# Performance work log

Measured on AMD Instinct MI355X. Metric: run time of the kernel, lower is better.

## Reference

```python
import jax, jax.numpy as jnp
import numpy as np

N, E = 100000, 1600000
IN_DIM, H, D = 128, 4, 32
ALPHA = 0.2  # leaky relu negative slope


def setup_inputs() -> dict:
    key = jax.random.key(0)
    k1, k2, k3, k4, k5, k6 = jax.random.split(key, 6)
    return {
        "inputs": jax.random.normal(k1, (N, IN_DIM), dtype=jnp.float32),
        "src": jax.random.randint(k2, (E,), 0, N, dtype=jnp.int32),
        "dst": jax.random.randint(k3, (E,), 0, N, dtype=jnp.int32),
        "fc_w": jax.random.normal(k4, (IN_DIM, H * D), dtype=jnp.float32) * (1.414 / np.sqrt(IN_DIM)),
        "attn_l": jax.random.normal(k5, (D,), dtype=jnp.float32) * 0.1,
        "attn_r": jax.random.normal(k6, (D,), dtype=jnp.float32) * 0.1,
    }


def reference(inputs, src, dst, fc_w, attn_l, attn_r):
    # fc + reshape to (N, H, D); feat_drop is identity (p=0)
    ft = (inputs @ fc_w).reshape(N, H, D)
    # attn_l/attn_r are (1,1,D) in torch -> broadcast over heads
    a1 = jnp.einsum("nhd,d->nh", ft, attn_l)  # (N, H)
    a2 = jnp.einsum("nhd,d->nh", ft, attn_r)  # (N, H)
    # per-edge logits; original keeps ONLY head-0 scores after edge_softmax
    # (scores[:, 0, :].unsqueeze(1)), so we only need head 0 here.
    e = jax.nn.leaky_relu(a1[src, 0] + a2[dst, 0], ALPHA)  # (E,)
    # numerically-stable segment softmax over destination nodes
    emax = jax.ops.segment_max(e, dst, num_segments=N)
    ex = jnp.exp(e - emax[dst])
    denom = jax.ops.segment_sum(ex, dst, num_segments=N)
    a = ex / denom[dst]  # (E,) broadcast to all heads
    # u_mul_e + sum aggregation; attn_drop is identity (p=0)
    msg = ft[src] * a[:, None, None]  # (E, H, D)
    out = jax.ops.segment_sum(msg, dst, num_segments=N)  # (N, H, D)
    return out
```

## Files before the change

### kernel.cpp

```cpp
#include <hip/hip_runtime.h>


#define ALPHA 0.2f
#define NBLK 512
#define BBITS 8
#define BSIZE 256
#define CAP 5120
#define ESLOTS 1024

typedef __attribute__((ext_vector_type(8))) short bf16x8;
typedef __attribute__((ext_vector_type(8))) unsigned short u16x8;
typedef __attribute__((ext_vector_type(4))) float f32x4;

__device__ __forceinline__ unsigned short f2bf(float f) {
    unsigned u = __float_as_uint(f);
    unsigned r = (u + 0x7FFFu + ((u >> 16) & 1u)) >> 16;
    return (unsigned short)r;
}

__global__ __launch_bounds__(256) void prep_kernel(const float* __restrict__ W,
                                                   u16x8* __restrict__ Wswz) {
    int gt = blockIdx.x * 256 + threadIdx.x;
    if (gt < 2048) {
        int n = gt >> 4, c = gt & 15;
        u16x8 v;
        #pragma unroll
        for (int j = 0; j < 8; ++j) v[j] = f2bf(W[(c * 8 + j) * 128 + n]);
        Wswz[n * 16 + (c ^ (n & 7))] = v;
    }
}

__global__ __launch_bounds__(256) void front_kernel(
        const float* __restrict__ A, const u16x8* __restrict__ Wswz,
        const float* __restrict__ attn_l, const float* __restrict__ attn_r,
        unsigned short* __restrict__ ftb,
        float* __restrict__ s_l, float* __restrict__ s_r, int N, int GB,
        const int* __restrict__ dst, unsigned* __restrict__ bh,
        int E, int nbucket, int slice) {
    __shared__ char smem[32768];
    const int tid = threadIdx.x;

    if (blockIdx.x >= (unsigned)GB) {
        unsigned* cnt = (unsigned*)smem;
        for (int i = tid; i < nbucket; i += 256) cnt[i] = 0u;
        __syncthreads();
        const int b = blockIdx.x - GB;
        int s0 = b * slice, s1 = min(s0 + slice, E);
        for (int i = s0 + tid; i < s1; i += 256)
            atomicAdd(&cnt[((unsigned)dst[i]) >> BBITS], 1u);
        __syncthreads();
        for (int k = tid; k < nbucket; k += 256)
            bh[(size_t)k * NBLK + b] = cnt[k];
        return;
    }

    u16x8* W_lds = (u16x8*)smem;
    const int block_row = blockIdx.x * 64;

    for (int i = tid; i < 2048; i += 256) W_lds[i] = Wswz[i];

    const int wv = tid >> 6;
    const int lane = tid & 63;
    const int lm = lane & 15;
    const int quad = lane >> 4;
    const int am = block_row + wv * 16 + lm;
    const bool rowok = (am < N);

    bf16x8 a_frag[4];
    #pragma unroll
    for (int ks = 0; ks < 4; ++ks) {
        int c = ks * 4 + quad;
        float4 v0 = make_float4(0.f, 0.f, 0.f, 0.f), v1 = v0;
        if (rowok) {
            const float4* p = (const float4*)(A + (size_t)am * 128 + c * 8);
            v0 = p[0]; v1 = p[1];
        }
        u16x8 u;
        u[0] = f2bf(v0.x); u[1] = f2bf(v0.y); u[2] = f2bf(v0.z); u[3] = f2bf(v0.w);
        u[4] = f2bf(v1.x); u[5] = f2bf(v1.y); u[6] = f2bf(v1.z); u[7] = f2bf(v1.w);
        a_frag[ks] = *(const bf16x8*)&u;
    }
    __syncthreads();

    f32x4 acc[8];
    #pragma unroll
    for (int t = 0; t < 8; ++t) acc[t] = (f32x4)(0.f);

    #pragma unroll
    for (int ks = 0; ks < 4; ++ks) {
        int c = ks * 4 + quad;
        #pragma unroll
        for (int t = 0; t < 8; ++t) {
            int n = t * 16 + lm;
            bf16x8 bf = *(const bf16x8*)&W_lds[n * 16 + (c ^ (n & 7))];
            acc[t] = __builtin_amdgcn_mfma_f32_16x16x32_bf16(a_frag[ks], bf, acc[t], 0, 0, 0);
        }
    }

    {
        float al0 = attn_l[lm], al1 = attn_l[16 + lm];
        float ar0 = attn_r[lm], ar1 = attn_r[16 + lm];
        #pragma unroll
        for (int r = 0; r < 4; ++r) {
            float pl = acc[0][r] * al0 + acc[1][r] * al1;
            float pr = acc[0][r] * ar0 + acc[1][r] * ar1;
            #pragma unroll
            for (int mask = 1; mask < 16; mask <<= 1) {
                pl += __shfl_xor(pl, mask, 64);
                pr += __shfl_xor(pr, mask, 64);
            }
            if (lm == 0) {
                int row = block_row + wv * 16 + quad * 4 + r;
                if (row < N) { s_l[row] = pl; s_r[row] = pr; }
            }
        }
    }

    __syncthreads();
    unsigned short* C_lds = (unsigned short*)smem;
    #pragma unroll
    for (int t = 0; t < 8; ++t) {
        #pragma unroll
        for (int r = 0; r < 4; ++r) {
            int mrow = wv * 16 + quad * 4 + r;
            C_lds[mrow * 128 + t * 16 + lm] = f2bf(acc[t][r]);
        }
    }
    __syncthreads();
    for (int l = tid; l < 1024; l += 256) {
        int m = l >> 4, c = l & 15;
        int row = block_row + m;
        if (row < N)
            *(u16x8*)(ftb + (size_t)row * 128 + c * 8) = *(const u16x8*)&C_lds[m * 128 + c * 8];
    }
}

__global__ __launch_bounds__(256) void scan1_kernel(const unsigned* __restrict__ counts,
                                                    unsigned* __restrict__ S,
                                                    unsigned* __restrict__ partials, int M) {
    __shared__ unsigned sh[256];
    const int tid = threadIdx.x;
    const int base = blockIdx.x * 1024 + tid * 4;
    unsigned v[4];
    unsigned s = 0;
    #pragma unroll
    for (int k = 0; k < 4; ++k) {
        int idx = base + k;
        v[k] = (idx < M) ? counts[idx] : 0u;
        s += v[k];
    }
    sh[tid] = s;
    __syncthreads();
    for (int off = 1; off < 256; off <<= 1) {
        unsigned t = (tid >= off) ? sh[tid - off] : 0u;
        __syncthreads();
        sh[tid] += t;
        __syncthreads();
    }
    if (tid == 255) partials[blockIdx.x] = sh[255];
    unsigned run = (tid == 0) ? 0u : sh[tid - 1];
    #pragma unroll
    for (int k = 0; k < 4; ++k) {
        int idx = base + k;
        if (idx < M) S[idx] = run;
        run += v[k];
    }
}

__global__ __launch_bounds__(256) void scan2_kernel(unsigned* __restrict__ partials, int NB) {
    __shared__ unsigned sh[256];
    const int tid = threadIdx.x;
    unsigned v[4];
    unsigned s = 0;
    #pragma unroll
    for (int k = 0; k < 4; ++k) {
        int idx = tid * 4 + k;
        v[k] = (idx < NB) ? partials[idx] : 0u;
        s += v[k];
    }
    sh[tid] = s;
    __syncthreads();
    for (int off = 1; off < 256; off <<= 1) {
        unsigned t = (tid >= off) ? sh[tid - off] : 0u;
        __syncthreads();
        sh[tid] += t;
        __syncthreads();
    }
    unsigned run = (tid == 0) ? 0u : sh[tid - 1];
    #pragma unroll
    for (int k = 0; k < 4; ++k) {
        int idx = tid * 4 + k;
        if (idx < NB) partials[idx] = run;
        run += v[k];
    }
}

__global__ __launch_bounds__(256) void bscatter_kernel(
        const int* __restrict__ src, const int* __restrict__ dst,
        const float* __restrict__ s_l, const float* __restrict__ s_r,
        const unsigned* __restrict__ S, const unsigned* __restrict__ partials,
        uint2* __restrict__ staged, int E, int nbucket, int slice) {
    __shared__ unsigned basel[512];
    __shared__ unsigned cur[512];
    const int b = blockIdx.x;
    for (int k = threadIdx.x; k < nbucket; k += 256) {
        unsigned idx = (unsigned)k * NBLK + b;
        basel[k] = S[idx] + partials[idx >> 10];
        cur[k] = 0u;
    }
    __syncthreads();
    int s0 = b * slice, s1 = min(s0 + slice, E);
    for (int i = s0 + threadIdx.x; i < s1; i += 256) {
        int s = src[i], d = dst[i];
        unsigned k = ((unsigned)d) >> BBITS;
        float x = s_l[s] + s_r[d];
        float e = (x > 0.f) ? x : ALPHA * x;
        unsigned pos = basel[k] + atomicAdd(&cur[k], 1u);
        staged[pos] = make_uint2((unsigned)s | (((unsigned)d & (BSIZE - 1)) << 20),
                                 __float_as_uint(e));
    }
}

__global__ __launch_bounds__(256) void bsort_kernel(
        uint2* __restrict__ staged, const unsigned* __restrict__ S,
        const unsigned* __restrict__ partials,
        unsigned* __restrict__ offsets, int N, int E, int nbucket) {
    __shared__ uint2 rec[CAP];
    __shared__ unsigned cnt[BSIZE], incl[BSIZE], cur[BSIZE];
    const int k = blockIdx.x;
    const int t = threadIdx.x;
    unsigned idx0 = (unsigned)k * NBLK;
    unsigned gstart = S[idx0] + partials[idx0 >> 10];
    unsigned gend = (k + 1 == nbucket) ? (unsigned)E
                                       : (S[idx0 + NBLK] + partials[(idx0 + NBLK) >> 10]);
    int n = (int)(gend - gstart);
    if (n > CAP) n = CAP;

    cnt[t] = 0u;
    __syncthreads();
    for (int i = t; i < n; i += 256)
        atomicAdd(&cnt[staged[gstart + i].x >> 20], 1u);
    __syncthreads();
    incl[t] = cnt[t];
    __syncthreads();
    for (int off = 1; off < 256; off <<= 1) {
        unsigned u = (t >= off) ? incl[t - off] : 0u;
        __syncthreads();
        incl[t] += u;
        __syncthreads();
    }
    cur[t] = 0u;
    __syncthreads();
    for (int i = t; i < n; i += 256) {
        uint2 r = staged[gstart + i];
        unsigned dl = r.x >> 20;
        unsigned p = incl[dl] - cnt[dl] + atomicAdd(&cur[dl], 1u);
        rec[p] = r;
    }
    __syncthreads();
    int d = k * BSIZE + t;
    if (d < N) {
        int b0 = (int)(incl[t] - cnt[t]);
        int c = (int)cnt[t];
        float m = -1e30f;
        for (int j = 0; j < c; ++j) m = fmaxf(m, __uint_as_float(rec[b0 + j].y));
        float sum = 0.f;
        for (int j = 0; j < c; ++j) sum += __expf(__uint_as_float(rec[b0 + j].y) - m);
        float rden = (c > 0) ? 1.f / sum : 0.f;
        for (int j = 0; j < c; ++j) {
            float a = __expf(__uint_as_float(rec[b0 + j].y) - m) * rden;
            rec[b0 + j].y = __float_as_uint(a);
        }
        offsets[d] = gstart + incl[t];
    }
    __syncthreads();
    for (int i = t; i < n; i += 256) {
        uint2 r = rec[i];
        staged[gstart + i] = make_uint2(r.x & 0xFFFFFu, r.y);
    }
}

__global__ __launch_bounds__(256) void aggregate_kernel(
        const uint2* __restrict__ edata, const unsigned* __restrict__ offsets,
        const unsigned short* __restrict__ ftb, float* __restrict__ out, int N) {
    __shared__ uint2 elds[ESLOTS];
    const int wv = threadIdx.x >> 6;
    const int lane = threadIdx.x & 63;
    const int eh = lane >> 4;
    const int j  = lane & 15;
    const int db = blockIdx.x * 4;
    const int d = db + wv;

    const unsigned bstart = (db == 0) ? 0u : offsets[db - 1];
    const unsigned bend = offsets[min(db + 3, N - 1)];
    unsigned start = 0u, end = 0u;
    if (d < N) {
        start = (d == 0) ? 0u : offsets[d - 1];
        end = offsets[d];
    }

    float acc[8] = {0.f, 0.f, 0.f, 0.f, 0.f, 0.f, 0.f, 0.f};

    for (unsigned cbase = bstart; cbase < bend; cbase += ESLOTS) {
        const unsigned cn = min((unsigned)ESLOTS, bend - cbase);
        __syncthreads();
        for (unsigned i = threadIdx.x; i < cn; i += 256)
            elds[i] = edata[cbase + i];
        __syncthreads();
        const unsigned lo = (start > cbase) ? start : cbase;
        const unsigned hi = (end < cbase + cn) ? end : (cbase + cn);
        for (unsigned e = lo; e < hi; e += 16) {
            unsigned i0 = e + eh, i1 = e + 4 + eh, i2 = e + 8 + eh, i3 = e + 12 + eh;
            uint2 e0 = (i0 < hi) ? elds[i0 - cbase] : make_uint2(0u, 0u);
            uint2 e1 = (i1 < hi) ? elds[i1 - cbase] : make_uint2(0u, 0u);
            uint2 e2 = (i2 < hi) ? elds[i2 - cbase] : make_uint2(0u, 0u);
            uint2 e3 = (i3 < hi) ? elds[i3 - cbase] : make_uint2(0u, 0u);
            uint4 q0 = *(const uint4*)(ftb + (size_t)e0.x * 128 + j * 8);
            uint4 q1 = *(const uint4*)(ftb + (size_t)e1.x * 128 + j * 8);
            uint4 q2 = *(const uint4*)(ftb + (size_t)e2.x * 128 + j * 8);
            uint4 q3 = *(const uint4*)(ftb + (size_t)e3.x * 128 + j * 8);
            float a0 = __uint_as_float(e0.y);
            float a1 = __uint_as_float(e1.y);
            float a2 = __uint_as_float(e2.y);
            float a3 = __uint_as_float(e3.y);
            const unsigned* w0 = (const unsigned*)&q0;
            const unsigned* w1 = (const unsigned*)&q1;
            const unsigned* w2 = (const unsigned*)&q2;
            const unsigned* w3 = (const unsigned*)&q3;
            #pragma unroll
            for (int p = 0; p < 4; ++p) {
                acc[2 * p]     += a0 * __uint_as_float(w0[p] << 16);
                acc[2 * p + 1] += a0 * __uint_as_float(w0[p] & 0xFFFF0000u);
                acc[2 * p]     += a1 * __uint_as_float(w1[p] << 16);
                acc[2 * p + 1] += a1 * __uint_as_float(w1[p] & 0xFFFF0000u);
                acc[2 * p]     += a2 * __uint_as_float(w2[p] << 16);
                acc[2 * p + 1] += a2 * __uint_as_float(w2[p] & 0xFFFF0000u);
                acc[2 * p]     += a3 * __uint_as_float(w3[p] << 16);
                acc[2 * p + 1] += a3 * __uint_as_float(w3[p] & 0xFFFF0000u);
            }
        }
    }
    #pragma unroll
    for (int p = 0; p < 8; ++p) {
        acc[p] += __shfl_xor(acc[p], 16, 64);
        acc[p] += __shfl_xor(acc[p], 32, 64);
    }
    if (d < N && eh == 0) {
        float4* op = (float4*)(out + (size_t)d * 128 + j * 8);
        op[0] = make_float4(acc[0], acc[1], acc[2], acc[3]);
        op[1] = make_float4(acc[4], acc[5], acc[6], acc[7]);
    }
}

static inline size_t align256(size_t x) { return (x + 255) & ~(size_t)255; }

extern "C" void kernel_launch(void* const* d_in, const int* in_sizes, int n_in,
                              void* d_out, int out_size, void* d_ws, size_t ws_size,
                              hipStream_t stream) {
    const float* inputs = (const float*)d_in[0];
    const int*   src    = (const int*)d_in[1];
    const int*   dst    = (const int*)d_in[2];
    const float* fc_w   = (const float*)d_in[3];
    const float* attn_l = (const float*)d_in[4];
    const float* attn_r = (const float*)d_in[5];
    float* out = (float*)d_out;

    const int N = in_sizes[0] / 128;
    const int E = in_sizes[1];
    const int nbucket = (N + BSIZE - 1) / BSIZE;
    const int M = nbucket * NBLK;
    const int NB1 = (M + 1023) / 1024;
    const int slice = (E + NBLK - 1) / NBLK;
    const int GB = (N + 63) / 64;

    char* w = (char*)d_ws;
    unsigned short* ftb = (unsigned short*)w;  w += align256((size_t)N * 128 * 2);
    float*    s_l      = (float*)w;     w += align256((size_t)N * 4);
    float*    s_r      = (float*)w;     w += align256((size_t)N * 4);
    unsigned* bh       = (unsigned*)w;  w += align256((size_t)M * 4);
    unsigned* S        = (unsigned*)w;  w += align256((size_t)M * 4);
    unsigned* partials = (unsigned*)w;  w += align256(1024 * 4);
    unsigned* offsets  = (unsigned*)w;  w += align256((size_t)N * 4);
    u16x8*    Wswz     = (u16x8*)w;     w += align256(2048 * 16);
    uint2*    staged   = (uint2*)w;     w += align256((size_t)E * 8);

    prep_kernel<<<8, 256, 0, stream>>>(fc_w, Wswz);
    front_kernel<<<GB + NBLK, 256, 0, stream>>>(inputs, Wswz, attn_l, attn_r,
                                                ftb, s_l, s_r, N, GB,
                                                dst, bh, E, nbucket, slice);
    scan1_kernel<<<NB1, 256, 0, stream>>>(bh, S, partials, M);
    scan2_kernel<<<1, 256, 0, stream>>>(partials, NB1);
    bscatter_kernel<<<NBLK, 256, 0, stream>>>(src, dst, s_l, s_r, S, partials,
                                              staged, E, nbucket, slice);
    bsort_kernel<<<nbucket, 256, 0, stream>>>(staged, S, partials, offsets,
                                              N, E, nbucket);
    aggregate_kernel<<<(N + 3) / 4, 256, 0, stream>>>(staged, offsets, ftb, out, N);
}
```

Measured before the change: 246.8 us.

## Fuse bucket sort, segment softmax and aggregation into one kernel

```diff
diff --git a/kernel.cpp b/kernel.cpp
--- a/kernel.cpp
+++ b/kernel.cpp
@@ -3,10 +3,10 @@
 
 #define ALPHA 0.2f
 #define NBLK 512
-#define BBITS 8
-#define BSIZE 256
-#define CAP 5120
-#define ESLOTS 1024
+#define BBITS 6
+#define BSIZE 64
+#define MAXBKT 1600
+#define CAP 1536
 
 typedef __attribute__((ext_vector_type(8))) short bf16x8;
 typedef __attribute__((ext_vector_type(8))) unsigned short u16x8;
@@ -200,8 +200,8 @@
         const float* __restrict__ s_l, const float* __restrict__ s_r,
         const unsigned* __restrict__ S, const unsigned* __restrict__ partials,
         uint2* __restrict__ staged, int E, int nbucket, int slice) {
-    __shared__ unsigned basel[512];
-    __shared__ unsigned cur[512];
+    __shared__ unsigned basel[MAXBKT];
+    __shared__ unsigned cur[MAXBKT];
     const int b = blockIdx.x;
     for (int k = threadIdx.x; k < nbucket; k += 256) {
         unsigned idx = (unsigned)k * NBLK + b;
@@ -221,10 +221,12 @@
     }
 }
 
-__global__ __launch_bounds__(256) void bsort_kernel(
-        uint2* __restrict__ staged, const unsigned* __restrict__ S,
+__global__ __launch_bounds__(256) void aggsort_kernel(
+        const uint2* __restrict__ staged, const unsigned* __restrict__ S,
         const unsigned* __restrict__ partials,
-        unsigned* __restrict__ offsets, int N, int E, int nbucket) {
+        const unsigned short* __restrict__ ftb, float* __restrict__ out,
+        int N, int E, int nbucket) {
+    __shared__ uint2 raw[CAP];
     __shared__ uint2 rec[CAP];
     __shared__ unsigned cnt[BSIZE], incl[BSIZE], cur[BSIZE];
     const int k = blockIdx.x;
@@ -236,119 +238,97 @@
     int n = (int)(gend - gstart);
     if (n > CAP) n = CAP;
 
-    cnt[t] = 0u;
-    __syncthreads();
-    for (int i = t; i < n; i += 256)
-        atomicAdd(&cnt[staged[gstart + i].x >> 20], 1u);
-    __syncthreads();
-    incl[t] = cnt[t];
-    __syncthreads();
-    for (int off = 1; off < 256; off <<= 1) {
-        unsigned u = (t >= off) ? incl[t - off] : 0u;
-        __syncthreads();
-        incl[t] += u;
-        __syncthreads();
-    }
-    cur[t] = 0u;
+    if (t < BSIZE) { cnt[t] = 0u; cur[t] = 0u; }
     __syncthreads();
     for (int i = t; i < n; i += 256) {
         uint2 r = staged[gstart + i];
+        raw[i] = r;
+        atomicAdd(&cnt[r.x >> 20], 1u);
+    }
+    __syncthreads();
+    if (t < BSIZE) incl[t] = cnt[t];
+    __syncthreads();
+    for (int off = 1; off < BSIZE; off <<= 1) {
+        unsigned u = (t < BSIZE && t >= off) ? incl[t - off] : 0u;
+        __syncthreads();
+        if (t < BSIZE) incl[t] += u;
+        __syncthreads();
+    }
+    for (int i = t; i < n; i += 256) {
+        uint2 r = raw[i];
         unsigned dl = r.x >> 20;
         unsigned p = incl[dl] - cnt[dl] + atomicAdd(&cur[dl], 1u);
-        rec[p] = r;
-    }
-    __syncthreads();
-    int d = k * BSIZE + t;
-    if (d < N) {
-        int b0 = (int)(incl[t] - cnt[t]);
-        int c = (int)cnt[t];
-        float m = -1e30f;
-        for (int j = 0; j < c; ++j) m = fmaxf(m, __uint_as_float(rec[b0 + j].y));
-        float sum = 0.f;
-        for (int j = 0; j < c; ++j) sum += __expf(__uint_as_float(rec[b0 + j].y) - m);
-        float rden = (c > 0) ? 1.f / sum : 0.f;
-        for (int j = 0; j < c; ++j) {
-            float a = __expf(__uint_as_float(rec[b0 + j].y) - m) * rden;
-            rec[b0 + j].y = __float_as_uint(a);
-        }
-        offsets[d] = gstart + incl[t];
-    }
-    __syncthreads();
-    for (int i = t; i < n; i += 256) {
-        uint2 r = rec[i];
-        staged[gstart + i] = make_uint2(r.x & 0xFFFFFu, r.y);
-    }
-}
-
-__global__ __launch_bounds__(256) void aggregate_kernel(
-        const uint2* __restrict__ edata, const unsigned* __restrict__ offsets,
-        const unsigned short* __restrict__ ftb, float* __restrict__ out, int N) {
-    __shared__ uint2 elds[ESLOTS];
-    const int wv = threadIdx.x >> 6;
-    const int lane = threadIdx.x & 63;
+        rec[p] = make_uint2(r.x & 0xFFFFFu, r.y);
+    }
+    __syncthreads();
+
+    const int wv = t >> 6;
+    const int lane = t & 63;
     const int eh = lane >> 4;
     const int j  = lane & 15;
-    const int db = blockIdx.x * 4;
-    const int d = db + wv;
-
-    const unsigned bstart = (db == 0) ? 0u : offsets[db - 1];
-    const unsigned bend = offsets[min(db + 3, N - 1)];
-    unsigned start = 0u, end = 0u;
-    if (d < N) {
-        start = (d == 0) ? 0u : offsets[d - 1];
-        end = offsets[d];
-    }
-
-    float acc[8] = {0.f, 0.f, 0.f, 0.f, 0.f, 0.f, 0.f, 0.f};
-
-    for (unsigned cbase = bstart; cbase < bend; cbase += ESLOTS) {
-        const unsigned cn = min((unsigned)ESLOTS, bend - cbase);
-        __syncthreads();
-        for (unsigned i = threadIdx.x; i < cn; i += 256)
-            elds[i] = edata[cbase + i];
-        __syncthreads();
-        const unsigned lo = (start > cbase) ? start : cbase;
-        const unsigned hi = (end < cbase + cn) ? end : (cbase + cn);
-        for (unsigned e = lo; e < hi; e += 16) {
-            unsigned i0 = e + eh, i1 = e + 4 + eh, i2 = e + 8 + eh, i3 = e + 12 + eh;
-            uint2 e0 = (i0 < hi) ? elds[i0 - cbase] : make_uint2(0u, 0u);
-            uint2 e1 = (i1 < hi) ? elds[i1 - cbase] : make_uint2(0u, 0u);
-            uint2 e2 = (i2 < hi) ? elds[i2 - cbase] : make_uint2(0u, 0u);
-            uint2 e3 = (i3 < hi) ? elds[i3 - cbase] : make_uint2(0u, 0u);
-            uint4 q0 = *(const uint4*)(ftb + (size_t)e0.x * 128 + j * 8);
-            uint4 q1 = *(const uint4*)(ftb + (size_t)e1.x * 128 + j * 8);
-            uint4 q2 = *(const uint4*)(ftb + (size_t)e2.x * 128 + j * 8);
-            uint4 q3 = *(const uint4*)(ftb + (size_t)e3.x * 128 + j * 8);
-            float a0 = __uint_as_float(e0.y);
-            float a1 = __uint_as_float(e1.y);
-            float a2 = __uint_as_float(e2.y);
-            float a3 = __uint_as_float(e3.y);
-            const unsigned* w0 = (const unsigned*)&q0;
-            const unsigned* w1 = (const unsigned*)&q1;
-            const unsigned* w2 = (const unsigned*)&q2;
-            const unsigned* w3 = (const unsigned*)&q3;
-            #pragma unroll
-            for (int p = 0; p < 4; ++p) {
-                acc[2 * p]     += a0 * __uint_as_float(w0[p] << 16);
-                acc[2 * p + 1] += a0 * __uint_as_float(w0[p] & 0xFFFF0000u);
-                acc[2 * p]     += a1 * __uint_as_float(w1[p] << 16);
-                acc[2 * p + 1] += a1 * __uint_as_float(w1[p] & 0xFFFF0000u);
-                acc[2 * p]     += a2 * __uint_as_float(w2[p] << 16);
-                acc[2 * p + 1] += a2 * __uint_as_float(w2[p] & 0xFFFF0000u);
-                acc[2 * p]     += a3 * __uint_as_float(w3[p] << 16);
-                acc[2 * p + 1] += a3 * __uint_as_float(w3[p] & 0xFFFF0000u);
+    for (int dd = 0; dd < 16; ++dd) {
+        const int ld = wv * 16 + dd;
+        const int d = k * BSIZE + ld;
+        if (d >= N) break;
+        const int b0 = (int)(incl[ld] - cnt[ld]);
+        const int c = (int)cnt[ld];
+        float acc[8] = {0.f, 0.f, 0.f, 0.f, 0.f, 0.f, 0.f, 0.f};
+        if (c > 0) {
+            float m = -1e30f;
+            for (int i = eh; i < c; i += 4)
+                m = fmaxf(m, __uint_as_float(rec[b0 + i].y));
+            m = fmaxf(m, __shfl_xor(m, 16, 64));
+            m = fmaxf(m, __shfl_xor(m, 32, 64));
+            float s = 0.f;
+            for (int i = eh; i < c; i += 4) {
+                float w = __expf(__uint_as_float(rec[b0 + i].y) - m);
+                s += w;
+                if (j == 0) rec[b0 + i].y = __float_as_uint(w);
             }
-        }
-    }
-    #pragma unroll
-    for (int p = 0; p < 8; ++p) {
-        acc[p] += __shfl_xor(acc[p], 16, 64);
-        acc[p] += __shfl_xor(acc[p], 32, 64);
-    }
-    if (d < N && eh == 0) {
-        float4* op = (float4*)(out + (size_t)d * 128 + j * 8);
-        op[0] = make_float4(acc[0], acc[1], acc[2], acc[3]);
-        op[1] = make_float4(acc[4], acc[5], acc[6], acc[7]);
+            s += __shfl_xor(s, 16, 64);
+            s += __shfl_xor(s, 32, 64);
+            const float rden = 1.f / s;
+            for (int e = 0; e < c; e += 16) {
+                int i0 = e + eh, i1 = i0 + 4, i2 = i0 + 8, i3 = i0 + 12;
+                uint2 e0 = (i0 < c) ? rec[b0 + i0] : make_uint2(0u, 0u);
+                uint2 e1 = (i1 < c) ? rec[b0 + i1] : make_uint2(0u, 0u);
+                uint2 e2 = (i2 < c) ? rec[b0 + i2] : make_uint2(0u, 0u);
+                uint2 e3 = (i3 < c) ? rec[b0 + i3] : make_uint2(0u, 0u);
+                uint4 q0 = *(const uint4*)(ftb + (size_t)e0.x * 128 + j * 8);
+                uint4 q1 = *(const uint4*)(ftb + (size_t)e1.x * 128 + j * 8);
+                uint4 q2 = *(const uint4*)(ftb + (size_t)e2.x * 128 + j * 8);
+                uint4 q3 = *(const uint4*)(ftb + (size_t)e3.x * 128 + j * 8);
+                float a0 = __uint_as_float(e0.y) * rden;
+                float a1 = __uint_as_float(e1.y) * rden;
+                float a2 = __uint_as_float(e2.y) * rden;
+                float a3 = __uint_as_float(e3.y) * rden;
+                const unsigned* w0 = (const unsigned*)&q0;
+                const unsigned* w1 = (const unsigned*)&q1;
+                const unsigned* w2 = (const unsigned*)&q2;
+                const unsigned* w3 = (const unsigned*)&q3;
+                #pragma unroll
+                for (int p = 0; p < 4; ++p) {
+                    acc[2 * p]     += a0 * __uint_as_float(w0[p] << 16);
+                    acc[2 * p + 1] += a0 * __uint_as_float(w0[p] & 0xFFFF0000u);
+                    acc[2 * p]     += a1 * __uint_as_float(w1[p] << 16);
+                    acc[2 * p + 1] += a1 * __uint_as_float(w1[p] & 0xFFFF0000u);
+                    acc[2 * p]     += a2 * __uint_as_float(w2[p] << 16);
+                    acc[2 * p + 1] += a2 * __uint_as_float(w2[p] & 0xFFFF0000u);
+                    acc[2 * p]     += a3 * __uint_as_float(w3[p] << 16);
+                    acc[2 * p + 1] += a3 * __uint_as_float(w3[p] & 0xFFFF0000u);
+                }
+            }
+        }
+        #pragma unroll
+        for (int p = 0; p < 8; ++p) {
+            acc[p] += __shfl_xor(acc[p], 16, 64);
+            acc[p] += __shfl_xor(acc[p], 32, 64);
+        }
+        if (eh == 0) {
+            float4* op = (float4*)(out + (size_t)d * 128 + j * 8);
+            op[0] = make_float4(acc[0], acc[1], acc[2], acc[3]);
+            op[1] = make_float4(acc[4], acc[5], acc[6], acc[7]);
+        }
     }
 }
 
@@ -380,7 +360,6 @@
     unsigned* bh       = (unsigned*)w;  w += align256((size_t)M * 4);
     unsigned* S        = (unsigned*)w;  w += align256((size_t)M * 4);
     unsigned* partials = (unsigned*)w;  w += align256(1024 * 4);
-    unsigned* offsets  = (unsigned*)w;  w += align256((size_t)N * 4);
     u16x8*    Wswz     = (u16x8*)w;     w += align256(2048 * 16);
     uint2*    staged   = (uint2*)w;     w += align256((size_t)E * 8);
 
@@ -392,7 +371,6 @@
     scan2_kernel<<<1, 256, 0, stream>>>(partials, NB1);
     bscatter_kernel<<<NBLK, 256, 0, stream>>>(src, dst, s_l, s_r, S, partials,
                                               staged, E, nbucket, slice);
-    bsort_kernel<<<nbucket, 256, 0, stream>>>(staged, S, partials, offsets,
-                                              N, E, nbucket);
-    aggregate_kernel<<<(N + 3) / 4, 256, 0, stream>>>(staged, offsets, ftb, out, N);
-}
+    aggsort_kernel<<<nbucket, 256, 0, stream>>>(staged, S, partials,
+                                                ftb, out, N, E, nbucket);
+}
```

Result: slower. 276.7 us (+12.1%).

## Fold weight prep and partials scan into consumer kernels, vectorize aggregate FMAs

Applied to the files above, without the earlier changes.

```diff
diff --git a/kernel.cpp b/kernel.cpp
--- a/kernel.cpp
+++ b/kernel.cpp
@@ -11,6 +11,7 @@
 typedef __attribute__((ext_vector_type(8))) short bf16x8;
 typedef __attribute__((ext_vector_type(8))) unsigned short u16x8;
 typedef __attribute__((ext_vector_type(4))) float f32x4;
+typedef __attribute__((ext_vector_type(2))) float f32x2;
 
 __device__ __forceinline__ unsigned short f2bf(float f) {
     unsigned u = __float_as_uint(f);
@@ -18,20 +19,8 @@
     return (unsigned short)r;
 }
 
-__global__ __launch_bounds__(256) void prep_kernel(const float* __restrict__ W,
-                                                   u16x8* __restrict__ Wswz) {
-    int gt = blockIdx.x * 256 + threadIdx.x;
-    if (gt < 2048) {
-        int n = gt >> 4, c = gt & 15;
-        u16x8 v;
-        #pragma unroll
-        for (int j = 0; j < 8; ++j) v[j] = f2bf(W[(c * 8 + j) * 128 + n]);
-        Wswz[n * 16 + (c ^ (n & 7))] = v;
-    }
-}
-
 __global__ __launch_bounds__(256) void front_kernel(
-        const float* __restrict__ A, const u16x8* __restrict__ Wswz,
+        const float* __restrict__ A, const float* __restrict__ W,
         const float* __restrict__ attn_l, const float* __restrict__ attn_r,
         unsigned short* __restrict__ ftb,
         float* __restrict__ s_l, float* __restrict__ s_r, int N, int GB,
@@ -57,7 +46,13 @@
     u16x8* W_lds = (u16x8*)smem;
     const int block_row = blockIdx.x * 64;
 
-    for (int i = tid; i < 2048; i += 256) W_lds[i] = Wswz[i];
+    for (int i = tid; i < 2048; i += 256) {
+        int n = i & 127, c = i >> 7;
+        u16x8 v;
+        #pragma unroll
+        for (int j = 0; j < 8; ++j) v[j] = f2bf(W[(c * 8 + j) * 128 + n]);
+        W_lds[n * 16 + (c ^ (n & 7))] = v;
+    }
 
     const int wv = tid >> 6;
     const int lane = tid & 63;
@@ -167,50 +162,42 @@
     }
 }
 
-__global__ __launch_bounds__(256) void scan2_kernel(unsigned* __restrict__ partials, int NB) {
-    __shared__ unsigned sh[256];
-    const int tid = threadIdx.x;
-    unsigned v[4];
-    unsigned s = 0;
-    #pragma unroll
-    for (int k = 0; k < 4; ++k) {
-        int idx = tid * 4 + k;
-        v[k] = (idx < NB) ? partials[idx] : 0u;
-        s += v[k];
-    }
-    sh[tid] = s;
+__device__ __forceinline__ void local_pscan(const unsigned* __restrict__ partials,
+                                            unsigned* pscan, int NB, int tid) {
+    unsigned pv = (tid < NB) ? partials[tid] : 0u;
+    pscan[tid] = pv;
     __syncthreads();
     for (int off = 1; off < 256; off <<= 1) {
-        unsigned t = (tid >= off) ? sh[tid - off] : 0u;
-        __syncthreads();
-        sh[tid] += t;
-        __syncthreads();
-    }
-    unsigned run = (tid == 0) ? 0u : sh[tid - 1];
-    #pragma unroll
-    for (int k = 0; k < 4; ++k) {
-        int idx = tid * 4 + k;
-        if (idx < NB) partials[idx] = run;
-        run += v[k];
-    }
+        unsigned t = (tid >= off) ? pscan[tid - off] : 0u;
+        __syncthreads();
+        pscan[tid] += t;
+        __syncthreads();
+    }
+    unsigned excl = (tid == 0) ? 0u : pscan[tid - 1];
+    __syncthreads();
+    pscan[tid] = excl;
+    __syncthreads();
 }
 
 __global__ __launch_bounds__(256) void bscatter_kernel(
         const int* __restrict__ src, const int* __restrict__ dst,
         const float* __restrict__ s_l, const float* __restrict__ s_r,
         const unsigned* __restrict__ S, const unsigned* __restrict__ partials,
-        uint2* __restrict__ staged, int E, int nbucket, int slice) {
+        uint2* __restrict__ staged, int E, int nbucket, int slice, int NB) {
+    __shared__ unsigned pscan[256];
     __shared__ unsigned basel[512];
     __shared__ unsigned cur[512];
     const int b = blockIdx.x;
-    for (int k = threadIdx.x; k < nbucket; k += 256) {
+    const int tid = threadIdx.x;
+    local_pscan(partials, pscan, NB, tid);
+    for (int k = tid; k < nbucket; k += 256) {
         unsigned idx = (unsigned)k * NBLK + b;
-        basel[k] = S[idx] + partials[idx >> 10];
+        basel[k] = S[idx] + pscan[idx >> 10];
         cur[k] = 0u;
     }
     __syncthreads();
     int s0 = b * slice, s1 = min(s0 + slice, E);
-    for (int i = s0 + threadIdx.x; i < s1; i += 256) {
+    for (int i = s0 + tid; i < s1; i += 256) {
         int s = src[i], d = dst[i];
         unsigned k = ((unsigned)d) >> BBITS;
         float x = s_l[s] + s_r[d];
@@ -224,15 +211,17 @@
 __global__ __launch_bounds__(256) void bsort_kernel(
         uint2* __restrict__ staged, const unsigned* __restrict__ S,
         const unsigned* __restrict__ partials,
-        unsigned* __restrict__ offsets, int N, int E, int nbucket) {
+        unsigned* __restrict__ offsets, int N, int E, int nbucket, int NB) {
     __shared__ uint2 rec[CAP];
+    __shared__ unsigned pscan[256];
     __shared__ unsigned cnt[BSIZE], incl[BSIZE], cur[BSIZE];
     const int k = blockIdx.x;
     const int t = threadIdx.x;
+    local_pscan(partials, pscan, NB, t);
     unsigned idx0 = (unsigned)k * NBLK;
-    unsigned gstart = S[idx0] + partials[idx0 >> 10];
+    unsigned gstart = S[idx0] + pscan[idx0 >> 10];
     unsigned gend = (k + 1 == nbucket) ? (unsigned)E
-                                       : (S[idx0 + NBLK] + partials[(idx0 + NBLK) >> 10]);
+                                       : (S[idx0 + NBLK] + pscan[(idx0 + NBLK) >> 10]);
     int n = (int)(gend - gstart);
     if (n > CAP) n = CAP;
 
@@ -299,7 +288,9 @@
         end = offsets[d];
     }
 
-    float acc[8] = {0.f, 0.f, 0.f, 0.f, 0.f, 0.f, 0.f, 0.f};
+    f32x2 acc2[4];
+    #pragma unroll
+    for (int p = 0; p < 4; ++p) acc2[p] = (f32x2)(0.f);
 
     for (unsigned cbase = bstart; cbase < bend; cbase += ESLOTS) {
         const unsigned cn = min((unsigned)ESLOTS, bend - cbase);
@@ -315,10 +306,10 @@
             uint2 e1 = (i1 < hi) ? elds[i1 - cbase] : make_uint2(0u, 0u);
             uint2 e2 = (i2 < hi) ? elds[i2 - cbase] : make_uint2(0u, 0u);
             uint2 e3 = (i3 < hi) ? elds[i3 - cbase] : make_uint2(0u, 0u);
-            uint4 q0 = *(const uint4*)(ftb + (size_t)e0.x * 128 + j * 8);
-            uint4 q1 = *(const uint4*)(ftb + (size_t)e1.x * 128 + j * 8);
-            uint4 q2 = *(const uint4*)(ftb + (size_t)e2.x * 128 + j * 8);
-            uint4 q3 = *(const uint4*)(ftb + (size_t)e3.x * 128 + j * 8);
+            uint4 q0 = *(const uint4*)(ftb + ((unsigned)(e0.x << 7) + (j << 3)));
+            uint4 q1 = *(const uint4*)(ftb + ((unsigned)(e1.x << 7) + (j << 3)));
+            uint4 q2 = *(const uint4*)(ftb + ((unsigned)(e2.x << 7) + (j << 3)));
+            uint4 q3 = *(const uint4*)(ftb + ((unsigned)(e3.x << 7) + (j << 3)));
             float a0 = __uint_as_float(e0.y);
             float a1 = __uint_as_float(e1.y);
             float a2 = __uint_as_float(e2.y);
@@ -329,17 +320,20 @@
             const unsigned* w3 = (const unsigned*)&q3;
             #pragma unroll
             for (int p = 0; p < 4; ++p) {
-                acc[2 * p]     += a0 * __uint_as_float(w0[p] << 16);
-                acc[2 * p + 1] += a0 * __uint_as_float(w0[p] & 0xFFFF0000u);
-                acc[2 * p]     += a1 * __uint_as_float(w1[p] << 16);
-                acc[2 * p + 1] += a1 * __uint_as_float(w1[p] & 0xFFFF0000u);
-                acc[2 * p]     += a2 * __uint_as_float(w2[p] << 16);
-                acc[2 * p + 1] += a2 * __uint_as_float(w2[p] & 0xFFFF0000u);
-                acc[2 * p]     += a3 * __uint_as_float(w3[p] << 16);
-                acc[2 * p + 1] += a3 * __uint_as_float(w3[p] & 0xFFFF0000u);
+                f32x2 v0 = { __uint_as_float(w0[p] << 16), __uint_as_float(w0[p] & 0xFFFF0000u) };
+                f32x2 v1 = { __uint_as_float(w1[p] << 16), __uint_as_float(w1[p] & 0xFFFF0000u) };
+                f32x2 v2 = { __uint_as_float(w2[p] << 16), __uint_as_float(w2[p] & 0xFFFF0000u) };
+                f32x2 v3 = { __uint_as_float(w3[p] << 16), __uint_as_float(w3[p] & 0xFFFF0000u) };
+                acc2[p] += v0 * a0;
+                acc2[p] += v1 * a1;
+                acc2[p] += v2 * a2;
+                acc2[p] += v3 * a3;
             }
         }
     }
+    float acc[8];
+    #pragma unroll
+    for (int p = 0; p < 4; ++p) { acc[2 * p] = acc2[p][0]; acc[2 * p + 1] = acc2[p][1]; }
     #pragma unroll
     for (int p = 0; p < 8; ++p) {
         acc[p] += __shfl_xor(acc[p], 16, 64);
@@ -381,18 +375,15 @@
     unsigned* S        = (unsigned*)w;  w += align256((size_t)M * 4);
     unsigned* partials = (unsigned*)w;  w += align256(1024 * 4);
     unsigned* offsets  = (unsigned*)w;  w += align256((size_t)N * 4);
-    u16x8*    Wswz     = (u16x8*)w;     w += align256(2048 * 16);
     uint2*    staged   = (uint2*)w;     w += align256((size_t)E * 8);
 
-    prep_kernel<<<8, 256, 0, stream>>>(fc_w, Wswz);
-    front_kernel<<<GB + NBLK, 256, 0, stream>>>(inputs, Wswz, attn_l, attn_r,
+    front_kernel<<<GB + NBLK, 256, 0, stream>>>(inputs, fc_w, attn_l, attn_r,
                                                 ftb, s_l, s_r, N, GB,
                                                 dst, bh, E, nbucket, slice);
     scan1_kernel<<<NB1, 256, 0, stream>>>(bh, S, partials, M);
-    scan2_kernel<<<1, 256, 0, stream>>>(partials, NB1);
     bscatter_kernel<<<NBLK, 256, 0, stream>>>(src, dst, s_l, s_r, S, partials,
-                                              staged, E, nbucket, slice);
+                                              staged, E, nbucket, slice, NB1);
     bsort_kernel<<<nbucket, 256, 0, stream>>>(staged, S, partials, offsets,
-                                              N, E, nbucket);
+                                              N, E, nbucket, NB1);
     aggregate_kernel<<<(N + 3) / 4, 256, 0, stream>>>(staged, offsets, ftb, out, N);
 }
```

Result: no change. 247.6 us (+0.3%).
